# Kernel optimization log

Measured on AMD Instinct MI355X. Metric: run time of the kernel, lower is better.

Reference implementation:

```python
import jax, jax.numpy as jnp
import numpy as np

EPS = 1e-5

def _layernorm(x, w, b):
    mu = jnp.mean(x, axis=-1, keepdims=True)
    var = jnp.mean(jnp.square(x - mu), axis=-1, keepdims=True)
    return (x - mu) * jax.lax.rsqrt(var + EPS) * w + b

def setup_inputs() -> dict:
    key = jax.random.key(0)
    ks = jax.random.split(key, 16)
    B, N, CZ, C = 1, 384, 128, 128
    s_z = 1.0 / np.sqrt(CZ)
    s_c = 1.0 / np.sqrt(C)
    inp = {
        "pair": jax.random.normal(ks[0], (B, N, N, CZ), jnp.float32),
        "ln_pair_w": jnp.ones((CZ,), jnp.float32),
        "ln_pair_b": jnp.zeros((CZ,), jnp.float32),
        "ln_out_w": jnp.ones((C,), jnp.float32),
        "ln_out_b": jnp.zeros((C,), jnp.float32),
        "g1_w": jax.random.uniform(ks[1], (C, CZ), jnp.float32, -s_z, s_z),
        "g1_b": jax.random.uniform(ks[2], (C,), jnp.float32, -s_z, s_z),
        "g2_w": jax.random.uniform(ks[3], (C, CZ), jnp.float32, -s_z, s_z),
        "g2_b": jax.random.uniform(ks[4], (C,), jnp.float32, -s_z, s_z),
        "l1_w": jax.random.uniform(ks[5], (C, CZ), jnp.float32, -s_z, s_z),
        "l1_b": jax.random.uniform(ks[6], (C,), jnp.float32, -s_z, s_z),
        "l2_w": jax.random.uniform(ks[7], (C, CZ), jnp.float32, -s_z, s_z),
        "l2_b": jax.random.uniform(ks[8], (C,), jnp.float32, -s_z, s_z),
        "gate_w": jax.random.uniform(ks[9], (CZ, CZ), jnp.float32, -s_z, s_z),
        "gate_b": jax.random.uniform(ks[10], (CZ,), jnp.float32, -s_z, s_z),
        "out_w": jax.random.uniform(ks[11], (CZ, C), jnp.float32, -s_c, s_c),
        "out_b": jax.random.uniform(ks[12], (CZ,), jnp.float32, -s_c, s_c),
    }
    return inp

def reference(pair, ln_pair_w, ln_pair_b, ln_out_w, ln_out_b,
              g1_w, g1_b, g2_w, g2_b, l1_w, l1_b, l2_w, l2_b,
              gate_w, gate_b, out_w, out_b):
    z = _layernorm(pair, ln_pair_w, ln_pair_b)                    # [B,N,N,cz]
    A = jax.nn.sigmoid(z @ g1_w.T + g1_b) * (z @ l1_w.T + l1_b)  # [B,N,N,c]
    Bm = jax.nn.sigmoid(z @ g2_w.T + g2_b) * (z @ l2_w.T + l2_b) # [B,N,N,c]
    G = jax.nn.sigmoid(z @ gate_w.T + gate_b)                     # [B,N,N,cz]
    vals = jnp.einsum('bikc,bjkc->bijc', A, Bm)                   # [B,N,N,c]
    out = G * (_layernorm(vals, ln_out_w, ln_out_b) @ out_w.T + out_b)
    return out
```

## Files before the change

### kernel.cpp

```cpp
#include <hip/hip_runtime.h>
#include <hip/hip_fp16.h>

#define NDIM 384
#define NN   147456
#define CZC  128

typedef _Float16 f16x8 __attribute__((ext_vector_type(8)));
typedef float    f32x4 __attribute__((ext_vector_type(4)));

static __device__ __forceinline__ unsigned short f2h(float f) {
  return __builtin_bit_cast(unsigned short, __float2half(f));
}
static __device__ __forceinline__ float h2f(unsigned short s) {
  return __half2float(__builtin_bit_cast(__half, s));
}
static __device__ __forceinline__ unsigned pk2(float lo, float hi) {
  return (unsigned)f2h(lo) | ((unsigned)f2h(hi) << 16);
}
static __device__ __forceinline__ float sigmoidf_(float x) {
  return __builtin_amdgcn_rcpf(1.0f + __expf(-x));
}

__global__ void k0_conv(const float* __restrict__ g1, const float* __restrict__ l1,
                        const float* __restrict__ g2, const float* __restrict__ l2,
                        const float* __restrict__ gw, const float* __restrict__ ow,
                        unsigned short* __restrict__ Wh)
{
  const int m = blockIdx.x >> 6;
  const float* s = (m == 0) ? g1 : (m == 1) ? l1 : (m == 2) ? g2 : (m == 3) ? l2
                 : (m == 4) ? gw : ow;
  const int e = (blockIdx.x & 63) * 256 + threadIdx.x;
  Wh[m * 16384 + e] = f2h(s[e]);
}

__global__ __launch_bounds__(256, 4) void k1_proj(
    const float* __restrict__ pair, const float* __restrict__ lnw, const float* __restrict__ lnb,
    const unsigned short* __restrict__ Wh,
    const float* __restrict__ g1b, const float* __restrict__ l1b,
    const float* __restrict__ g2b, const float* __restrict__ l2b,
    const float* __restrict__ gtb,
    unsigned short* __restrict__ Ah, unsigned short* __restrict__ Bh,
    unsigned short* __restrict__ G)
{
  __shared__ char zb[16384];
  __shared__ char sb[16384];
  const int t  = threadIdx.x;
  const int r0 = blockIdx.x * 64;

  {
    const int rl = t >> 2, quad = t & 3, c0 = quad * 32;
    const float4* src = reinterpret_cast<const float4*>(pair + (size_t)(r0 + rl) * CZC + c0);
    float v[32];
    float s = 0.f, ss = 0.f;
#pragma unroll
    for (int q = 0; q < 8; ++q) {
      float4 f4 = src[q];
      v[4*q] = f4.x; v[4*q+1] = f4.y; v[4*q+2] = f4.z; v[4*q+3] = f4.w;
    }
#pragma unroll
    for (int j = 0; j < 32; ++j) { s += v[j]; ss += v[j] * v[j]; }
    s  += __shfl_xor(s, 1);  s  += __shfl_xor(s, 2);
    ss += __shfl_xor(ss, 1); ss += __shfl_xor(ss, 2);
    const float mu   = s * (1.f / 128.f);
    const float rstd = rsqrtf(ss * (1.f / 128.f) - mu * mu + 1e-5f);
    unsigned u[16];
#pragma unroll
    for (int q = 0; q < 8; ++q) {
      float4 w4 = reinterpret_cast<const float4*>(lnw + c0)[q];
      float4 b4 = reinterpret_cast<const float4*>(lnb + c0)[q];
      float z0 = (v[4*q  ] - mu) * rstd * w4.x + b4.x;
      float z1 = (v[4*q+1] - mu) * rstd * w4.y + b4.y;
      float z2 = (v[4*q+2] - mu) * rstd * w4.z + b4.z;
      float z3 = (v[4*q+3] - mu) * rstd * w4.w + b4.w;
      u[2*q] = pk2(z0, z1); u[2*q+1] = pk2(z2, z3);
    }
#pragma unroll
    for (int g = 0; g < 4; ++g) {
      int gi = quad * 4 + g;
      *reinterpret_cast<uint4*>(zb + rl * 256 + 16 * (gi ^ (rl & 7))) =
          make_uint4(u[4*g], u[4*g+1], u[4*g+2], u[4*g+3]);
    }
  }
  __syncthreads();

  const int w = t >> 6, l = t & 63;
  const int lrow = l & 15, lk = l >> 4;
  const int colbase = w * 32;

  auto ldA = [&](int mt, int ks) -> f16x8 {
    int row = mt * 16 + lrow;
    int gi  = ks * 4 + lk;
    return *reinterpret_cast<const f16x8*>(zb + row * 256 + 16 * (gi ^ (row & 7)));
  };
  auto ldB = [&](const unsigned short* Wm, int nt, int ks) -> f16x8 {
    int col = colbase + nt * 16 + lrow;
    return *reinterpret_cast<const f16x8*>(Wm + col * 128 + ks * 32 + lk * 8);
  };
  auto flush = [&](unsigned short* Ot) {
#pragma unroll
    for (int q = 0; q < 4; ++q) {
      int i = t + 256 * q;
      int col = i >> 3, sl = i & 7;
      uint4 u = *reinterpret_cast<const uint4*>(sb + col * 128 + ((sl ^ (col & 7)) * 16));
      *reinterpret_cast<uint4*>(Ot + (size_t)col * NN + r0 + sl * 8) = u;
    }
  };
  auto stage = [&](int col, int mt, unsigned lo, unsigned hi) {
    int s16 = (mt * 2 + (lk >> 1)) ^ (col & 7);
    *reinterpret_cast<uint2*>(sb + col * 128 + s16 * 16 + (lk & 1) * 8) = make_uint2(lo, hi);
  };

  auto do_pair = [&](const unsigned short* Wg, const unsigned short* Wl,
                     const float* bgp, const float* blp, unsigned short* Ot) {
    f32x4 accg[4][2], accl[4][2];
#pragma unroll
    for (int mt = 0; mt < 4; ++mt)
#pragma unroll
      for (int nt = 0; nt < 2; ++nt) { accg[mt][nt] = 0.f; accl[mt][nt] = 0.f; }
#pragma unroll
    for (int ks = 0; ks < 4; ++ks) {
      f16x8 af[4];
#pragma unroll
      for (int mt = 0; mt < 4; ++mt) af[mt] = ldA(mt, ks);
#pragma unroll
      for (int nt = 0; nt < 2; ++nt) {
        f16x8 bg_ = ldB(Wg, nt, ks);
#pragma unroll
        for (int mt = 0; mt < 4; ++mt)
          accg[mt][nt] = __builtin_amdgcn_mfma_f32_16x16x32_f16(af[mt], bg_, accg[mt][nt], 0, 0, 0);
        f16x8 bl_ = ldB(Wl, nt, ks);
#pragma unroll
        for (int mt = 0; mt < 4; ++mt)
          accl[mt][nt] = __builtin_amdgcn_mfma_f32_16x16x32_f16(af[mt], bl_, accl[mt][nt], 0, 0, 0);
      }
    }
    __syncthreads();
#pragma unroll
    for (int mt = 0; mt < 4; ++mt)
#pragma unroll
      for (int nt = 0; nt < 2; ++nt) {
        int col = colbase + nt * 16 + lrow;
        float gb = bgp[col], lb = blp[col];
        float a0 = sigmoidf_(accg[mt][nt][0] + gb) * (accl[mt][nt][0] + lb);
        float a1 = sigmoidf_(accg[mt][nt][1] + gb) * (accl[mt][nt][1] + lb);
        float a2 = sigmoidf_(accg[mt][nt][2] + gb) * (accl[mt][nt][2] + lb);
        float a3 = sigmoidf_(accg[mt][nt][3] + gb) * (accl[mt][nt][3] + lb);
        stage(col, mt, pk2(a0, a1), pk2(a2, a3));
      }
    __syncthreads();
    flush(Ot);
  };

  do_pair(Wh + 0 * 16384, Wh + 1 * 16384, g1b, l1b, Ah);
  do_pair(Wh + 2 * 16384, Wh + 3 * 16384, g2b, l2b, Bh);

  if (G) {
    f32x4 acc[4][2];
#pragma unroll
    for (int mt = 0; mt < 4; ++mt)
#pragma unroll
      for (int nt = 0; nt < 2; ++nt) acc[mt][nt] = 0.f;
    const unsigned short* Wg = Wh + 4 * 16384;
#pragma unroll
    for (int ks = 0; ks < 4; ++ks) {
      f16x8 af[4];
#pragma unroll
      for (int mt = 0; mt < 4; ++mt) af[mt] = ldA(mt, ks);
#pragma unroll
      for (int nt = 0; nt < 2; ++nt) {
        f16x8 bf_ = ldB(Wg, nt, ks);
#pragma unroll
        for (int mt = 0; mt < 4; ++mt)
          acc[mt][nt] = __builtin_amdgcn_mfma_f32_16x16x32_f16(af[mt], bf_, acc[mt][nt], 0, 0, 0);
      }
    }
    __syncthreads();
#pragma unroll
    for (int mt = 0; mt < 4; ++mt)
#pragma unroll
      for (int nt = 0; nt < 2; ++nt) {
        int col = colbase + nt * 16 + lrow;
        float gb = gtb[col];
        stage(col, mt, pk2(sigmoidf_(acc[mt][nt][0] + gb), sigmoidf_(acc[mt][nt][1] + gb)),
                       pk2(sigmoidf_(acc[mt][nt][2] + gb), sigmoidf_(acc[mt][nt][3] + gb)));
      }
    __syncthreads();
    flush(G);
  }
}

__global__ __launch_bounds__(256) void k2_tri(
    const unsigned short* __restrict__ Ah, const unsigned short* __restrict__ Bh,
    unsigned short* __restrict__ v16)
{
  __shared__ char As[8192];
  __shared__ char Bs[8192];
  __shared__ char Vs[32768];
  const int x  = blockIdx.x & 7;
  const int r  = blockIdx.x >> 3;
  const int tt = r % 9;
  const int c  = (r / 9) * 8 + x;
  const int ib = (tt / 3) * 128, jb = (tt % 3) * 128;
  const size_t co = (size_t)c * NN;
  const int t = threadIdx.x, w = t >> 6, l = t & 63;
  const int wi = (w >> 1) * 64, wj = (w & 1) * 64;
  const int lrow = l & 15, lk = l >> 4;
  const int srow = t >> 2, sgr = t & 3;

  f32x4 acc[4][4];
#pragma unroll
  for (int mt = 0; mt < 4; ++mt)
#pragma unroll
    for (int nt = 0; nt < 4; ++nt) acc[mt][nt] = 0.f;

  for (int kb = 0; kb < 12; ++kb) {
    const size_t ka  = co + (size_t)(ib + srow) * NDIM + kb * 32 + sgr * 8;
    const size_t kb_ = co + (size_t)(jb + srow) * NDIM + kb * 32 + sgr * 8;
    uint4 a0 = *reinterpret_cast<const uint4*>(Ah + ka);
    uint4 a1 = *reinterpret_cast<const uint4*>(Ah + ka + 64 * NDIM);
    uint4 b0 = *reinterpret_cast<const uint4*>(Bh + kb_);
    uint4 b1 = *reinterpret_cast<const uint4*>(Bh + kb_ + 64 * NDIM);
    __syncthreads();
    const int g0 = 16 * (sgr ^ (srow & 3));
    *reinterpret_cast<uint4*>(As + srow * 64 + g0)        = a0;
    *reinterpret_cast<uint4*>(As + (srow + 64) * 64 + g0) = a1;
    *reinterpret_cast<uint4*>(Bs + srow * 64 + g0)        = b0;
    *reinterpret_cast<uint4*>(Bs + (srow + 64) * 64 + g0) = b1;
    __syncthreads();
    f16x8 af[4], bfr[4];
#pragma unroll
    for (int mt = 0; mt < 4; ++mt) {
      int row = wi + mt * 16 + lrow;
      af[mt] = *reinterpret_cast<const f16x8*>(As + row * 64 + 16 * (lk ^ (row & 3)));
    }
#pragma unroll
    for (int nt = 0; nt < 4; ++nt) {
      int row = wj + nt * 16 + lrow;
      bfr[nt] = *reinterpret_cast<const f16x8*>(Bs + row * 64 + 16 * (lk ^ (row & 3)));
    }
#pragma unroll
    for (int mt = 0; mt < 4; ++mt)
#pragma unroll
      for (int nt = 0; nt < 4; ++nt)
        acc[mt][nt] = __builtin_amdgcn_mfma_f32_16x16x32_f16(af[mt], bfr[nt], acc[mt][nt], 0, 0, 0);
  }

  __syncthreads();
#pragma unroll
  for (int mt = 0; mt < 4; ++mt)
#pragma unroll
    for (int nt = 0; nt < 4; ++nt) {
      const int j = wj + nt * 16 + lrow;
#pragma unroll
      for (int reg = 0; reg < 4; ++reg) {
        const int i = wi + mt * 16 + lk * 4 + reg;
        int sl = (j >> 3) ^ (i & 15);
        *reinterpret_cast<unsigned short*>(Vs + i * 256 + sl * 16 + (j & 7) * 2)
            = f2h(acc[mt][nt][reg]);
      }
    }
  __syncthreads();
  unsigned short* vc = v16 + co;
#pragma unroll
  for (int q = 0; q < 8; ++q) {
    int idx = t + 256 * q;
    int i = idx >> 4, sl = idx & 15;
    uint4 u = *reinterpret_cast<const uint4*>(Vs + i * 256 + ((sl ^ (i & 15)) * 16));
    *reinterpret_cast<uint4*>(vc + (size_t)(ib + i) * NDIM + jb + sl * 8) = u;
  }
}

__global__ __launch_bounds__(256, 3) void k3_out(
    const float* __restrict__ pair, const unsigned short* __restrict__ v16,
    const unsigned short* __restrict__ G,
    const float* __restrict__ lnpw, const float* __restrict__ lnpb,
    const float* __restrict__ lnow, const float* __restrict__ lnob,
    const unsigned short* __restrict__ Wh,
    const float* __restrict__ gtb, const float* __restrict__ outb,
    float* __restrict__ outp)
{
  __shared__ char smem[53248];
  unsigned short* vs = reinterpret_cast<unsigned short*>(smem);
  char* aux = smem + 18432;
  char* zvb = smem + 36864;
  const int t  = threadIdx.x;
  const int p0 = blockIdx.x * 64;

#pragma unroll
  for (int q = 0; q < 4; ++q) {
    int ci = t + 256 * q;
    int c = ci >> 3, ch8 = ci & 7;
    uint4 u = *reinterpret_cast<const uint4*>(v16 + (size_t)c * NN + p0 + ch8 * 8);
    int g = ch8 ^ (c & 7);
    *reinterpret_cast<uint4*>(vs + c * 72 + g * 8) = u;
  }
  if (G) {
    unsigned short* gs = reinterpret_cast<unsigned short*>(aux);
#pragma unroll
    for (int q = 0; q < 4; ++q) {
      int ci = t + 256 * q;
      int c = ci >> 3, ch8 = ci & 7;
      uint4 u = *reinterpret_cast<const uint4*>(G + (size_t)c * NN + p0 + ch8 * 8);
      int g = ch8 ^ (c & 7);
      *reinterpret_cast<uint4*>(gs + c * 72 + g * 8) = u;
    }
  } else {
    char* zgb = aux;
    const int rl = t >> 2, quad = t & 3, c0 = quad * 32;
    const float4* src = reinterpret_cast<const float4*>(pair + (size_t)(p0 + rl) * CZC + c0);
    float v[32];
    float s = 0.f, ss = 0.f;
#pragma unroll
    for (int q = 0; q < 8; ++q) {
      float4 f4 = src[q];
      v[4*q] = f4.x; v[4*q+1] = f4.y; v[4*q+2] = f4.z; v[4*q+3] = f4.w;
    }
#pragma unroll
    for (int j = 0; j < 32; ++j) { s += v[j]; ss += v[j] * v[j]; }
    s  += __shfl_xor(s, 1);  s  += __shfl_xor(s, 2);
    ss += __shfl_xor(ss, 1); ss += __shfl_xor(ss, 2);
    const float mu   = s * (1.f / 128.f);
    const float rstd = rsqrtf(ss * (1.f / 128.f) - mu * mu + 1e-5f);
    unsigned u[16];
#pragma unroll
    for (int q = 0; q < 8; ++q) {
      float4 w4 = reinterpret_cast<const float4*>(lnpw + c0)[q];
      float4 b4 = reinterpret_cast<const float4*>(lnpb + c0)[q];
      float z0 = (v[4*q  ] - mu) * rstd * w4.x + b4.x;
      float z1 = (v[4*q+1] - mu) * rstd * w4.y + b4.y;
      float z2 = (v[4*q+2] - mu) * rstd * w4.z + b4.z;
      float z3 = (v[4*q+3] - mu) * rstd * w4.w + b4.w;
      u[2*q] = pk2(z0, z1); u[2*q+1] = pk2(z2, z3);
    }
#pragma unroll
    for (int g = 0; g < 4; ++g) {
      int gi = quad * 4 + g;
      *reinterpret_cast<uint4*>(zgb + rl * 256 + 16 * (gi ^ (rl & 7))) =
          make_uint4(u[4*g], u[4*g+1], u[4*g+2], u[4*g+3]);
    }
  }
  __syncthreads();

  const int w = t >> 6, l = t & 63;
  const int lrow = l & 15, lk = l >> 4;
  const int colbase = w * 32;

  auto ldZ = [&](const char* base, int mt, int ks) -> f16x8 {
    int row = mt * 16 + lrow;
    int gi  = ks * 4 + lk;
    return *reinterpret_cast<const f16x8*>(base + row * 256 + 16 * (gi ^ (row & 7)));
  };
  auto ldW = [&](const unsigned short* Wm, int nt, int ks) -> f16x8 {
    int col = colbase + nt * 16 + lrow;
    return *reinterpret_cast<const f16x8*>(Wm + col * 128 + ks * 32 + lk * 8);
  };

  f32x4 gacc[4][2];
#pragma unroll
  for (int mt = 0; mt < 4; ++mt)
#pragma unroll
    for (int nt = 0; nt < 2; ++nt) gacc[mt][nt] = 0.f;
  if (!G) {
    const unsigned short* Wg = Wh + 4 * 16384;
#pragma unroll
    for (int ks = 0; ks < 4; ++ks) {
      f16x8 af[4];
#pragma unroll
      for (int mt = 0; mt < 4; ++mt) af[mt] = ldZ(aux, mt, ks);
#pragma unroll
      for (int nt = 0; nt < 2; ++nt) {
        f16x8 bf_ = ldW(Wg, nt, ks);
#pragma unroll
        for (int mt = 0; mt < 4; ++mt)
          gacc[mt][nt] = __builtin_amdgcn_mfma_f32_16x16x32_f16(af[mt], bf_, gacc[mt][nt], 0, 0, 0);
      }
    }
  }

  {
    const int pl = t >> 2, quad = t & 3, c0q = quad * 32;
    float v[32];
#pragma unroll
    for (int j = 0; j < 32; ++j) {
      int c = c0q + j;
      v[j] = h2f(vs[c * 72 + (((pl >> 3) ^ (c & 7)) << 3) + (pl & 7)]);
    }
    float s = 0.f, ss = 0.f;
#pragma unroll
    for (int j = 0; j < 32; ++j) { s += v[j]; ss += v[j] * v[j]; }
    s  += __shfl_xor(s, 1);  s  += __shfl_xor(s, 2);
    ss += __shfl_xor(ss, 1); ss += __shfl_xor(ss, 2);
    const float mu   = s * (1.f / 128.f);
    const float rstd = rsqrtf(ss * (1.f / 128.f) - mu * mu + 1e-5f);
    unsigned u[16];
#pragma unroll
    for (int q = 0; q < 8; ++q) {
      float4 w4 = reinterpret_cast<const float4*>(lnow + c0q)[q];
      float4 b4 = reinterpret_cast<const float4*>(lnob + c0q)[q];
      float z0 = (v[4*q  ] - mu) * rstd * w4.x + b4.x;
      float z1 = (v[4*q+1] - mu) * rstd * w4.y + b4.y;
      float z2 = (v[4*q+2] - mu) * rstd * w4.z + b4.z;
      float z3 = (v[4*q+3] - mu) * rstd * w4.w + b4.w;
      u[2*q] = pk2(z0, z1); u[2*q+1] = pk2(z2, z3);
    }
#pragma unroll
    for (int g = 0; g < 4; ++g) {
      int gi = quad * 4 + g;
      *reinterpret_cast<uint4*>(zvb + pl * 256 + 16 * (gi ^ (pl & 7))) =
          make_uint4(u[4*g], u[4*g+1], u[4*g+2], u[4*g+3]);
    }
  }
  __syncthreads();

  const unsigned short* Wo = Wh + 5 * 16384;
  const unsigned short* gs = reinterpret_cast<const unsigned short*>(aux);
  f32x4 acc[4][2];
#pragma unroll
  for (int mt = 0; mt < 4; ++mt)
#pragma unroll
    for (int nt = 0; nt < 2; ++nt) acc[mt][nt] = 0.f;
#pragma unroll
  for (int ks = 0; ks < 4; ++ks) {
    f16x8 af[4];
#pragma unroll
    for (int mt = 0; mt < 4; ++mt) af[mt] = ldZ(zvb, mt, ks);
#pragma unroll
    for (int nt = 0; nt < 2; ++nt) {
      f16x8 bf_ = ldW(Wo, nt, ks);
#pragma unroll
      for (int mt = 0; mt < 4; ++mt)
        acc[mt][nt] = __builtin_amdgcn_mfma_f32_16x16x32_f16(af[mt], bf_, acc[mt][nt], 0, 0, 0);
    }
  }
#pragma unroll
  for (int mt = 0; mt < 4; ++mt)
#pragma unroll
    for (int nt = 0; nt < 2; ++nt) {
      int cz = colbase + nt * 16 + lrow;
      float ob = outb[cz], gb = gtb[cz];
#pragma unroll
      for (int reg = 0; reg < 4; ++reg) {
        int plc = mt * 16 + lk * 4 + reg;
        float gv;
        if (G) gv = h2f(gs[cz * 72 + (((plc >> 3) ^ (cz & 7)) << 3) + (plc & 7)]);
        else   gv = sigmoidf_(gacc[mt][nt][reg] + gb);
        outp[(size_t)(p0 + plc) * CZC + cz] = gv * (acc[mt][nt][reg] + ob);
      }
    }
}

extern "C" void kernel_launch(void* const* d_in, const int* in_sizes, int n_in,
                              void* d_out, int out_size, void* d_ws, size_t ws_size,
                              hipStream_t stream)
{
  const float* pair      = (const float*)d_in[0];
  const float* ln_pair_w = (const float*)d_in[1];
  const float* ln_pair_b = (const float*)d_in[2];
  const float* ln_out_w  = (const float*)d_in[3];
  const float* ln_out_b  = (const float*)d_in[4];
  const float* g1_w      = (const float*)d_in[5];
  const float* g1_b      = (const float*)d_in[6];
  const float* g2_w      = (const float*)d_in[7];
  const float* g2_b      = (const float*)d_in[8];
  const float* l1_w      = (const float*)d_in[9];
  const float* l1_b      = (const float*)d_in[10];
  const float* l2_w      = (const float*)d_in[11];
  const float* l2_b      = (const float*)d_in[12];
  const float* gate_w    = (const float*)d_in[13];
  const float* gate_b    = (const float*)d_in[14];
  const float* out_w     = (const float*)d_in[15];
  const float* out_b     = (const float*)d_in[16];

  const size_t WH = 196608;
  const size_t H  = 37748736;
  char* ws  = (char*)d_ws;
  char* dob = (char*)d_out;

  unsigned short* Wp = (unsigned short*)ws;
  unsigned short* V  = (unsigned short*)(ws + WH);
  unsigned short* G  = (ws_size >= WH + 2 * H) ? (unsigned short*)(ws + WH + H) : nullptr;
  unsigned short* Ah = (unsigned short*)dob;
  unsigned short* Bh = (unsigned short*)(dob + H);

  k0_conv<<<384, 256, 0, stream>>>(g1_w, l1_w, g2_w, l2_w, gate_w, out_w, Wp);
  k1_proj<<<2304, 256, 0, stream>>>(pair, ln_pair_w, ln_pair_b, Wp,
                                    g1_b, l1_b, g2_b, l2_b, gate_b, Ah, Bh, G);
  k2_tri<<<1152, 256, 0, stream>>>(Ah, Bh, V);
  k3_out<<<2304, 256, 0, stream>>>(pair, V, G, ln_pair_w, ln_pair_b, ln_out_w, ln_out_b,
                                   Wp, gate_b, out_b, (float*)d_out);
}
```

Before: 187.9 us.

## Process 128 rows per block in projection kernel with XCD-aware row mapping

The projection kernel now handles 128 rows per block instead of 64, doubling the LDS tiles and halving the grid. Each wave reuses its weight fragments across two row halves, and the flush writes 256-byte contiguous runs per output column instead of 128. Block indices are remapped so each XCD covers a contiguous range of rows. The cost is lower occupancy (launch bounds go from 4 to 2 blocks, with more LDS per block) and fewer blocks to hide latency.

```diff
diff --git a/kernel.cpp b/kernel.cpp
--- a/kernel.cpp
+++ b/kernel.cpp
@@ -33,7 +33,7 @@
   Wh[m * 16384 + e] = f2h(s[e]);
 }
 
-__global__ __launch_bounds__(256, 4) void k1_proj(
+__global__ __launch_bounds__(256, 2) void k1_proj(
     const float* __restrict__ pair, const float* __restrict__ lnw, const float* __restrict__ lnb,
     const unsigned short* __restrict__ Wh,
     const float* __restrict__ g1b, const float* __restrict__ l1b,
@@ -42,43 +42,47 @@
     unsigned short* __restrict__ Ah, unsigned short* __restrict__ Bh,
     unsigned short* __restrict__ G)
 {
-  __shared__ char zb[16384];
-  __shared__ char sb[16384];
-  const int t  = threadIdx.x;
-  const int r0 = blockIdx.x * 64;
+  __shared__ char zb[32768];
+  __shared__ char sb[32768];
+  const int t   = threadIdx.x;
+  const int xcd = blockIdx.x & 7;
+  const int r0  = (xcd * 144 + (blockIdx.x >> 3)) * 128;
 
   {
     const int rl = t >> 2, quad = t & 3, c0 = quad * 32;
-    const float4* src = reinterpret_cast<const float4*>(pair + (size_t)(r0 + rl) * CZC + c0);
-    float v[32];
-    float s = 0.f, ss = 0.f;
-#pragma unroll
-    for (int q = 0; q < 8; ++q) {
-      float4 f4 = src[q];
-      v[4*q] = f4.x; v[4*q+1] = f4.y; v[4*q+2] = f4.z; v[4*q+3] = f4.w;
-    }
-#pragma unroll
-    for (int j = 0; j < 32; ++j) { s += v[j]; ss += v[j] * v[j]; }
-    s  += __shfl_xor(s, 1);  s  += __shfl_xor(s, 2);
-    ss += __shfl_xor(ss, 1); ss += __shfl_xor(ss, 2);
-    const float mu   = s * (1.f / 128.f);
-    const float rstd = rsqrtf(ss * (1.f / 128.f) - mu * mu + 1e-5f);
-    unsigned u[16];
-#pragma unroll
-    for (int q = 0; q < 8; ++q) {
-      float4 w4 = reinterpret_cast<const float4*>(lnw + c0)[q];
-      float4 b4 = reinterpret_cast<const float4*>(lnb + c0)[q];
-      float z0 = (v[4*q  ] - mu) * rstd * w4.x + b4.x;
-      float z1 = (v[4*q+1] - mu) * rstd * w4.y + b4.y;
-      float z2 = (v[4*q+2] - mu) * rstd * w4.z + b4.z;
-      float z3 = (v[4*q+3] - mu) * rstd * w4.w + b4.w;
-      u[2*q] = pk2(z0, z1); u[2*q+1] = pk2(z2, z3);
-    }
-#pragma unroll
-    for (int g = 0; g < 4; ++g) {
-      int gi = quad * 4 + g;
-      *reinterpret_cast<uint4*>(zb + rl * 256 + 16 * (gi ^ (rl & 7))) =
-          make_uint4(u[4*g], u[4*g+1], u[4*g+2], u[4*g+3]);
+    for (int b = 0; b < 2; ++b) {
+      const int row = b * 64 + rl;
+      const float4* src = reinterpret_cast<const float4*>(pair + (size_t)(r0 + row) * CZC + c0);
+      float v[32];
+      float s = 0.f, ss = 0.f;
+#pragma unroll
+      for (int q = 0; q < 8; ++q) {
+        float4 f4 = src[q];
+        v[4*q] = f4.x; v[4*q+1] = f4.y; v[4*q+2] = f4.z; v[4*q+3] = f4.w;
+      }
+#pragma unroll
+      for (int j = 0; j < 32; ++j) { s += v[j]; ss += v[j] * v[j]; }
+      s  += __shfl_xor(s, 1);  s  += __shfl_xor(s, 2);
+      ss += __shfl_xor(ss, 1); ss += __shfl_xor(ss, 2);
+      const float mu   = s * (1.f / 128.f);
+      const float rstd = rsqrtf(ss * (1.f / 128.f) - mu * mu + 1e-5f);
+      unsigned u[16];
+#pragma unroll
+      for (int q = 0; q < 8; ++q) {
+        float4 w4 = reinterpret_cast<const float4*>(lnw + c0)[q];
+        float4 b4 = reinterpret_cast<const float4*>(lnb + c0)[q];
+        float z0 = (v[4*q  ] - mu) * rstd * w4.x + b4.x;
+        float z1 = (v[4*q+1] - mu) * rstd * w4.y + b4.y;
+        float z2 = (v[4*q+2] - mu) * rstd * w4.z + b4.z;
+        float z3 = (v[4*q+3] - mu) * rstd * w4.w + b4.w;
+        u[2*q] = pk2(z0, z1); u[2*q+1] = pk2(z2, z3);
+      }
+#pragma unroll
+      for (int g = 0; g < 4; ++g) {
+        int gi = quad * 4 + g;
+        *reinterpret_cast<uint4*>(zb + row * 256 + 16 * (gi ^ (row & 7))) =
+            make_uint4(u[4*g], u[4*g+1], u[4*g+2], u[4*g+3]);
+      }
     }
   }
   __syncthreads();
@@ -87,8 +91,8 @@
   const int lrow = l & 15, lk = l >> 4;
   const int colbase = w * 32;
 
-  auto ldA = [&](int mt, int ks) -> f16x8 {
-    int row = mt * 16 + lrow;
+  auto ldA = [&](int h, int mt, int ks) -> f16x8 {
+    int row = h * 64 + mt * 16 + lrow;
     int gi  = ks * 4 + lk;
     return *reinterpret_cast<const f16x8*>(zb + row * 256 + 16 * (gi ^ (row & 7)));
   };
@@ -96,57 +100,61 @@
     int col = colbase + nt * 16 + lrow;
     return *reinterpret_cast<const f16x8*>(Wm + col * 128 + ks * 32 + lk * 8);
   };
+  auto stageh = [&](int col, int h, int mt, unsigned lo, unsigned hi) {
+    int gran = h * 8 + mt * 2 + (lk >> 1);
+    *reinterpret_cast<uint2*>(sb + col * 256 + 16 * (gran ^ (col & 15)) + (lk & 1) * 8)
+        = make_uint2(lo, hi);
+  };
   auto flush = [&](unsigned short* Ot) {
 #pragma unroll
-    for (int q = 0; q < 4; ++q) {
+    for (int q = 0; q < 8; ++q) {
       int i = t + 256 * q;
-      int col = i >> 3, sl = i & 7;
-      uint4 u = *reinterpret_cast<const uint4*>(sb + col * 128 + ((sl ^ (col & 7)) * 16));
+      int col = i >> 4, sl = i & 15;
+      uint4 u = *reinterpret_cast<const uint4*>(sb + col * 256 + 16 * (sl ^ (col & 15)));
       *reinterpret_cast<uint4*>(Ot + (size_t)col * NN + r0 + sl * 8) = u;
     }
-  };
-  auto stage = [&](int col, int mt, unsigned lo, unsigned hi) {
-    int s16 = (mt * 2 + (lk >> 1)) ^ (col & 7);
-    *reinterpret_cast<uint2*>(sb + col * 128 + s16 * 16 + (lk & 1) * 8) = make_uint2(lo, hi);
   };
 
   auto do_pair = [&](const unsigned short* Wg, const unsigned short* Wl,
                      const float* bgp, const float* blp, unsigned short* Ot) {
-    f32x4 accg[4][2], accl[4][2];
-#pragma unroll
-    for (int mt = 0; mt < 4; ++mt)
-#pragma unroll
-      for (int nt = 0; nt < 2; ++nt) { accg[mt][nt] = 0.f; accl[mt][nt] = 0.f; }
-#pragma unroll
-    for (int ks = 0; ks < 4; ++ks) {
-      f16x8 af[4];
-#pragma unroll
-      for (int mt = 0; mt < 4; ++mt) af[mt] = ldA(mt, ks);
-#pragma unroll
-      for (int nt = 0; nt < 2; ++nt) {
-        f16x8 bg_ = ldB(Wg, nt, ks);
-#pragma unroll
-        for (int mt = 0; mt < 4; ++mt)
-          accg[mt][nt] = __builtin_amdgcn_mfma_f32_16x16x32_f16(af[mt], bg_, accg[mt][nt], 0, 0, 0);
-        f16x8 bl_ = ldB(Wl, nt, ks);
-#pragma unroll
-        for (int mt = 0; mt < 4; ++mt)
-          accl[mt][nt] = __builtin_amdgcn_mfma_f32_16x16x32_f16(af[mt], bl_, accl[mt][nt], 0, 0, 0);
-      }
-    }
     __syncthreads();
 #pragma unroll
-    for (int mt = 0; mt < 4; ++mt)
-#pragma unroll
-      for (int nt = 0; nt < 2; ++nt) {
-        int col = colbase + nt * 16 + lrow;
-        float gb = bgp[col], lb = blp[col];
-        float a0 = sigmoidf_(accg[mt][nt][0] + gb) * (accl[mt][nt][0] + lb);
-        float a1 = sigmoidf_(accg[mt][nt][1] + gb) * (accl[mt][nt][1] + lb);
-        float a2 = sigmoidf_(accg[mt][nt][2] + gb) * (accl[mt][nt][2] + lb);
-        float a3 = sigmoidf_(accg[mt][nt][3] + gb) * (accl[mt][nt][3] + lb);
-        stage(col, mt, pk2(a0, a1), pk2(a2, a3));
-      }
+    for (int h = 0; h < 2; ++h) {
+      f32x4 accg[4][2], accl[4][2];
+#pragma unroll
+      for (int mt = 0; mt < 4; ++mt)
+#pragma unroll
+        for (int nt = 0; nt < 2; ++nt) { accg[mt][nt] = 0.f; accl[mt][nt] = 0.f; }
+#pragma unroll
+      for (int ks = 0; ks < 4; ++ks) {
+        f16x8 af[4];
+#pragma unroll
+        for (int mt = 0; mt < 4; ++mt) af[mt] = ldA(h, mt, ks);
+#pragma unroll
+        for (int nt = 0; nt < 2; ++nt) {
+          f16x8 bg_ = ldB(Wg, nt, ks);
+#pragma unroll
+          for (int mt = 0; mt < 4; ++mt)
+            accg[mt][nt] = __builtin_amdgcn_mfma_f32_16x16x32_f16(af[mt], bg_, accg[mt][nt], 0, 0, 0);
+          f16x8 bl_ = ldB(Wl, nt, ks);
+#pragma unroll
+          for (int mt = 0; mt < 4; ++mt)
+            accl[mt][nt] = __builtin_amdgcn_mfma_f32_16x16x32_f16(af[mt], bl_, accl[mt][nt], 0, 0, 0);
+        }
+      }
+#pragma unroll
+      for (int mt = 0; mt < 4; ++mt)
+#pragma unroll
+        for (int nt = 0; nt < 2; ++nt) {
+          int col = colbase + nt * 16 + lrow;
+          float gb = bgp[col], lb = blp[col];
+          float a0 = sigmoidf_(accg[mt][nt][0] + gb) * (accl[mt][nt][0] + lb);
+          float a1 = sigmoidf_(accg[mt][nt][1] + gb) * (accl[mt][nt][1] + lb);
+          float a2 = sigmoidf_(accg[mt][nt][2] + gb) * (accl[mt][nt][2] + lb);
+          float a3 = sigmoidf_(accg[mt][nt][3] + gb) * (accl[mt][nt][3] + lb);
+          stageh(col, h, mt, pk2(a0, a1), pk2(a2, a3));
+        }
+    }
     __syncthreads();
     flush(Ot);
   };
@@ -155,35 +163,39 @@
   do_pair(Wh + 2 * 16384, Wh + 3 * 16384, g2b, l2b, Bh);
 
   if (G) {
-    f32x4 acc[4][2];
-#pragma unroll
-    for (int mt = 0; mt < 4; ++mt)
-#pragma unroll
-      for (int nt = 0; nt < 2; ++nt) acc[mt][nt] = 0.f;
+    __syncthreads();
     const unsigned short* Wg = Wh + 4 * 16384;
 #pragma unroll
-    for (int ks = 0; ks < 4; ++ks) {
-      f16x8 af[4];
-#pragma unroll
-      for (int mt = 0; mt < 4; ++mt) af[mt] = ldA(mt, ks);
-#pragma unroll
-      for (int nt = 0; nt < 2; ++nt) {
-        f16x8 bf_ = ldB(Wg, nt, ks);
-#pragma unroll
-        for (int mt = 0; mt < 4; ++mt)
-          acc[mt][nt] = __builtin_amdgcn_mfma_f32_16x16x32_f16(af[mt], bf_, acc[mt][nt], 0, 0, 0);
-      }
-    }
-    __syncthreads();
-#pragma unroll
-    for (int mt = 0; mt < 4; ++mt)
-#pragma unroll
-      for (int nt = 0; nt < 2; ++nt) {
-        int col = colbase + nt * 16 + lrow;
-        float gb = gtb[col];
-        stage(col, mt, pk2(sigmoidf_(acc[mt][nt][0] + gb), sigmoidf_(acc[mt][nt][1] + gb)),
-                       pk2(sigmoidf_(acc[mt][nt][2] + gb), sigmoidf_(acc[mt][nt][3] + gb)));
-      }
+    for (int h = 0; h < 2; ++h) {
+      f32x4 acc[4][2];
+#pragma unroll
+      for (int mt = 0; mt < 4; ++mt)
+#pragma unroll
+        for (int nt = 0; nt < 2; ++nt) acc[mt][nt] = 0.f;
+#pragma unroll
+      for (int ks = 0; ks < 4; ++ks) {
+        f16x8 af[4];
+#pragma unroll
+        for (int mt = 0; mt < 4; ++mt) af[mt] = ldA(h, mt, ks);
+#pragma unroll
+        for (int nt = 0; nt < 2; ++nt) {
+          f16x8 bf_ = ldB(Wg, nt, ks);
+#pragma unroll
+          for (int mt = 0; mt < 4; ++mt)
+            acc[mt][nt] = __builtin_amdgcn_mfma_f32_16x16x32_f16(af[mt], bf_, acc[mt][nt], 0, 0, 0);
+        }
+      }
+#pragma unroll
+      for (int mt = 0; mt < 4; ++mt)
+#pragma unroll
+        for (int nt = 0; nt < 2; ++nt) {
+          int col = colbase + nt * 16 + lrow;
+          float gb = gtb[col];
+          stageh(col, h, mt,
+                 pk2(sigmoidf_(acc[mt][nt][0] + gb), sigmoidf_(acc[mt][nt][1] + gb)),
+                 pk2(sigmoidf_(acc[mt][nt][2] + gb), sigmoidf_(acc[mt][nt][3] + gb)));
+        }
+    }
     __syncthreads();
     flush(G);
   }
@@ -483,7 +495,7 @@
   unsigned short* Bh = (unsigned short*)(dob + H);
 
   k0_conv<<<384, 256, 0, stream>>>(g1_w, l1_w, g2_w, l2_w, gate_w, out_w, Wp);
-  k1_proj<<<2304, 256, 0, stream>>>(pair, ln_pair_w, ln_pair_b, Wp,
+  k1_proj<<<1152, 256, 0, stream>>>(pair, ln_pair_w, ln_pair_b, Wp,
                                     g1_b, l1_b, g2_b, l2_b, gate_b, Ah, Bh, G);
   k2_tri<<<1152, 256, 0, stream>>>(Ah, Bh, V);
   k3_out<<<2304, 256, 0, stream>>>(pair, V, G, ln_pair_w, ln_pair_b, ln_out_w, ln_out_b,
```

Measured after the change: 166.1 us. 11.6% less time.
